# Performance work log

Measured on AMD Instinct MI355X. Metric: run time of the kernel, lower is better.

Reference implementation:

```python
import jax, jax.numpy as jnp
import numpy as np


def setup_inputs() -> dict:
    key = jax.random.key(0)
    kh, ks, kwi, kwo, kcw = jax.random.split(key, 5)
    B = 2048        # decode batch (one token per request)
    H = 2048        # hidden_size
    K = 4           # conv kernel; L_cache = K - 1 = 3
    P = 8192        # req_to_token_pool size
    hidden_states = jax.random.normal(kh, (B, H), dtype=jnp.float32)
    conv_state = jax.random.normal(ks, (P, H, K - 1), dtype=jnp.float32)
    # unique, in-range pool slots (index_copy_ semantics need uniqueness)
    req_pool_indices = jnp.arange(B, dtype=jnp.int32)
    w_in = jax.random.normal(kwi, (3 * H, H), dtype=jnp.float32) * 0.02
    w_out = jax.random.normal(kwo, (H, H), dtype=jnp.float32) * 0.02
    conv_w = jax.random.normal(kcw, (H, K), dtype=jnp.float32) * 0.2
    return {
        "hidden_states": hidden_states,
        "conv_state": conv_state,
        "req_pool_indices": req_pool_indices,
        "w_in": w_in,
        "w_out": w_out,
        "conv_w": conv_w,
    }


def reference(hidden_states, conv_state, req_pool_indices, w_in, w_out, conv_w):
    """Lfm2ShortConv._forward_decode (conv_bias=False).

    Returns (y, new_conv_state) where new_conv_state is the scattered cache.
    """
    idx = req_pool_indices.astype(jnp.int32)
    # in_proj: [B, H] @ [H, 3H] -> [B, 3H]
    proj = hidden_states @ w_in.T
    B_gate, C_gate, x = jnp.split(proj, 3, axis=-1)
    Bx = B_gate * x                                  # [B, H]
    cur = conv_state[idx]                            # gather: [B, H, K-1]
    # sliding window: [old state (K-1 taps), newest token] -> [B, H, K]
    conv_in = jnp.concatenate([cur, Bx[:, :, None]], axis=-1)
    # depthwise causal conv as mul-sum over taps
    conv_out = jnp.einsum("bhk,hk->bh", conv_in, conv_w)
    y = (C_gate * conv_out) @ w_out.T                # [B, H]
    # scatter updated window (drop oldest tap)
    new_conv_state = conv_state.at[idx].set(conv_in[:, :, 1:])
    return y, new_conv_state
```

## Files before the change

### kernel.cpp

```cpp
#include <hip/hip_runtime.h>
#include <hip/hip_bf16.h>


typedef __bf16 bf16x8 __attribute__((ext_vector_type(8)));
typedef float f32x4 __attribute__((ext_vector_type(4)));

__device__ __forceinline__ unsigned short f2bf(float f) {
    union { float f; unsigned int u; } c; c.f = f;
    unsigned int u = c.u;
    u = u + 0x7FFFu + ((u >> 16) & 1u);
    return (unsigned short)(u >> 16);
}
__device__ __forceinline__ float bf2f(unsigned short u) {
    union { unsigned int i; float f; } c; c.i = ((unsigned int)u) << 16;
    return c.f;
}

__global__ void prep(const float4* __restrict__ hs, const float4* __restrict__ wi,
                     const float4* __restrict__ wo,
                     ushort4* __restrict__ hs_bf, ushort4* __restrict__ wi_bf,
                     ushort4* __restrict__ wo_bf,
                     float4* __restrict__ y,
                     int* __restrict__ inv, int P,
                     int n1, int n2, int n3, int n4) {
    int i = blockIdx.x * blockDim.x + threadIdx.x;
    if (i < P) inv[i] = -1;
    const float4* s; ushort4* d; int j = i;
    if (j < n1)            { s = hs; d = hs_bf; }
    else if ((j -= n1) < n2) { s = wi; d = wi_bf; }
    else if ((j -= n2) < n3) { s = wo; d = wo_bf; }
    else if ((j -= n3) < n4) { float4 z = {0.f, 0.f, 0.f, 0.f}; y[j] = z; return; }
    else return;
    float4 v = s[j];
    ushort4 o; o.x = f2bf(v.x); o.y = f2bf(v.y); o.z = f2bf(v.z); o.w = f2bf(v.w);
    d[j] = o;
}

__global__ void scatter_inv(const int* __restrict__ idx, int* __restrict__ inv, int B) {
    int b = blockIdx.x * blockDim.x + threadIdx.x;
    if (b < B) inv[idx[b]] = b;
}


#define GTILE 128
#define GBK 64

__device__ __forceinline__ void gl_lds16(const unsigned short* g, unsigned short* l) {
    __builtin_amdgcn_global_load_lds(
        (const __attribute__((address_space(1))) unsigned int*)g,
        (__attribute__((address_space(3))) unsigned int*)l,
        16, 0, 0);
}

template<int MODE>
__global__ __launch_bounds__(256) void gemm_bt(
    const unsigned short* __restrict__ A,
    const unsigned short* __restrict__ B,
    void* __restrict__ Cv,
    int M, int N, int K, int ksplit, int nbx,
    const float* __restrict__ cs_in,
    const int* __restrict__ inv,
    float* __restrict__ cs_out,
    int HL, int P, int NC)
{
    __shared__ __align__(16) unsigned short Asm[GTILE * GBK];
    __shared__ __align__(16) unsigned short Bsm[GTILE * GBK];

    int bm, bn, kb;
    if (MODE == 1) {
        int id = blockIdx.x;
        int q = id / 5, r = id % 5;
        if (r == 4) {
            for (int p = q; p < P; p += NC) {
                if (inv[p] >= 0) continue;
                const float4* s4 = (const float4*)(cs_in + (size_t)p * HL);
                float4* d4 = (float4*)(cs_out + (size_t)p * HL);
#pragma unroll
                for (int f = threadIdx.x; f < GTILE * 12; f += 256) d4[f] = s4[f];
            }
            return;
        }
        int gid = q * 4 + r;
        bn = (gid % nbx) * GTILE;
        bm = (gid / nbx) * GTILE;
        kb = 0;
    } else {
        bn = blockIdx.x * GTILE;
        bm = blockIdx.y * GTILE;
        kb = blockIdx.z * ksplit;
    }

    const int tid  = threadIdx.x;
    const int lane = tid & 63;
    const int wave = tid >> 6;
    const int quad = lane >> 4;
    const int l16  = lane & 15;

    const int wm = (wave >> 1) * 64;
    const int wn = (wave & 1) * 64;

    f32x4 acc[4][4] = {};

    const int sr = tid >> 3;
    const int scsw = (((tid & 7) ^ (sr & 7)) * 8);
    const unsigned short* Ag[4];
    const unsigned short* Bg[4];
#pragma unroll
    for (int k4 = 0; k4 < 4; k4++) {
        Ag[k4] = A + (size_t)(bm + k4 * 32 + sr) * K + scsw;
        Bg[k4] = B + (size_t)(bn + k4 * 32 + sr) * K + scsw;
    }

    for (int kt = kb; kt < kb + ksplit; kt += GBK) {
        __syncthreads();
#pragma unroll
        for (int k4 = 0; k4 < 4; k4++) {
            gl_lds16(Ag[k4] + kt, Asm + k4 * 2048 + wave * 512);
            gl_lds16(Bg[k4] + kt, Bsm + k4 * 2048 + wave * 512);
        }
        __syncthreads();

#pragma unroll
        for (int kk = 0; kk < 2; kk++) {
            bf16x8 a[4], b[4];
            const int csw = (kk * 32 + quad * 8) ^ ((l16 & 7) * 8);
#pragma unroll
            for (int i = 0; i < 4; i++)
                a[i] = *(const bf16x8*)&Asm[(wm + i * 16 + l16) * GBK + csw];
#pragma unroll
            for (int j = 0; j < 4; j++)
                b[j] = *(const bf16x8*)&Bsm[(wn + j * 16 + l16) * GBK + csw];
#pragma unroll
            for (int i = 0; i < 4; i++)
#pragma unroll
                for (int j = 0; j < 4; j++)
                    acc[i][j] = __builtin_amdgcn_mfma_f32_16x16x32_bf16(
                        a[i], b[j], acc[i][j], 0, 0, 0);
        }
    }

#pragma unroll
    for (int i = 0; i < 4; i++) {
#pragma unroll
        for (int j = 0; j < 4; j++) {
#pragma unroll
            for (int r = 0; r < 4; r++) {
                int row = bm + wm + i * 16 + quad * 4 + r;
                int col = bn + wn + j * 16 + l16;
                if (MODE == 1) {
                    ((unsigned short*)Cv)[(size_t)row * N + col] = f2bf(acc[i][j][r]);
                } else {
                    __hip_atomic_fetch_add((float*)Cv + (size_t)row * N + col,
                                           acc[i][j][r],
                                           __ATOMIC_RELAXED,
                                           __HIP_MEMORY_SCOPE_AGENT);
                }
            }
        }
    }
}

__global__ void elemwise(const unsigned short* __restrict__ proj,
                         const float* __restrict__ cs_in,
                         const int* __restrict__ idx,
                         const float* __restrict__ conv_w,
                         float* __restrict__ state_out,
                         unsigned short* __restrict__ g_bf,
                         int B, int H, int hshift, int hmask)
{
    int t = blockIdx.x * blockDim.x + threadIdx.x;
    if (t >= B * H) return;
    int b = t >> hshift;
    int h = t & hmask;
    int slot = idx[b];
    size_t prow = (size_t)b * 3 * H;
    float Bg = bf2f(proj[prow + h]);
    float Cg = bf2f(proj[prow + H + h]);
    float xv = bf2f(proj[prow + 2 * H + h]);
    float bx = Bg * xv;
    const float* cs = cs_in + ((size_t)slot * H + h) * 3;
    float c0 = cs[0], c1 = cs[1], c2 = cs[2];
    float4 cw = *(const float4*)(conv_w + 4 * h);
    float co = c0 * cw.x + c1 * cw.y + c2 * cw.z + bx * cw.w;
    float* so = state_out + ((size_t)slot * H + h) * 3;
    so[0] = c1; so[1] = c2; so[2] = bx;
    g_bf[t] = f2bf(Cg * co);
}

extern "C" void kernel_launch(void* const* d_in, const int* in_sizes, int n_in,
                              void* d_out, int out_size, void* d_ws, size_t ws_size,
                              hipStream_t stream) {
    const float* hs         = (const float*)d_in[0];
    const float* conv_state = (const float*)d_in[1];
    const int*   idx        = (const int*)d_in[2];
    const float* w_in       = (const float*)d_in[3];
    const float* w_out      = (const float*)d_in[4];
    const float* conv_w     = (const float*)d_in[5];

    const int B  = in_sizes[2];
    const int H  = in_sizes[0] / B;
    const int Kc = in_sizes[5] / H;
    const int Lc = Kc - 1;
    const int P  = (int)((long long)in_sizes[1] / ((long long)H * Lc));

    float* y_out     = (float*)d_out;
    float* state_out = y_out + (size_t)B * H;

    unsigned short* hs_bf    = (unsigned short*)d_ws;
    unsigned short* w_in_bf  = hs_bf + (size_t)B * H;
    unsigned short* w_out_bf = w_in_bf + (size_t)3 * H * H;
    unsigned short* proj_bf  = w_out_bf + (size_t)H * H;
    unsigned short* g_bf     = proj_bf + (size_t)B * 3 * H;
    int*            inv      = (int*)(g_bf + (size_t)B * H);

    const int thr = 256;

    {
        int n1 = B * H / 4, n2 = 3 * H * H / 4, n3 = H * H / 4, n4 = B * H / 4;
        int tot = n1 + n2 + n3 + n4;
        prep<<<(tot + thr - 1) / thr, thr, 0, stream>>>(
            (const float4*)hs, (const float4*)w_in, (const float4*)w_out,
            (ushort4*)hs_bf, (ushort4*)w_in_bf, (ushort4*)w_out_bf,
            (float4*)y_out, inv, P, n1, n2, n3, n4);
    }
    scatter_inv<<<(B + thr - 1) / thr, thr, 0, stream>>>(idx, inv, B);

    {
        int nbx = 3 * H / GTILE;
        int NG  = nbx * (B / GTILE);
        int NC  = NG / 4;
        gemm_bt<1><<<NG + NC, 256, 0, stream>>>(
            hs_bf, w_in_bf, proj_bf, B, 3 * H, H, H, nbx,
            conv_state, inv, state_out, 3 * H, P, NC);
    }

    {
        int hshift = 0; while ((1 << hshift) < H) hshift++;
        int n = B * H;
        elemwise<<<(n + thr - 1) / thr, thr, 0, stream>>>(
            proj_bf, conv_state, idx, conv_w, state_out, g_bf, B, H, hshift, H - 1);
    }

    {
        dim3 grid(H / GTILE, B / GTILE, 4);
        gemm_bt<0><<<grid, 256, 0, stream>>>(
            g_bf, w_out_bf, y_out, B, H, H, H / 4, H / GTILE,
            nullptr, nullptr, nullptr, 0, 0, 0);
    }
}
```

Before: 579.5 us.

## Replace atomic split-K accumulation with partial buffers and reduction; batch state copies

The second GEMM now splits K in two instead of four and writes plain float partials into a workspace buffer instead of using atomic adds. A separate kernel then sums the two partials into the output, so prep no longer has to zero y. The conv-state copy blocks now handle two pool rows per iteration, issuing all loads before the stores to raise memory-level parallelism. The trade-offs are an extra kernel launch and extra partial-buffer traffic, plus fewer blocks in the second GEMM.

```diff
diff --git a/kernel.cpp b/kernel.cpp
--- a/kernel.cpp
+++ b/kernel.cpp
@@ -20,16 +20,14 @@
                      const float4* __restrict__ wo,
                      ushort4* __restrict__ hs_bf, ushort4* __restrict__ wi_bf,
                      ushort4* __restrict__ wo_bf,
-                     float4* __restrict__ y,
                      int* __restrict__ inv, int P,
-                     int n1, int n2, int n3, int n4) {
+                     int n1, int n2, int n3) {
     int i = blockIdx.x * blockDim.x + threadIdx.x;
     if (i < P) inv[i] = -1;
     const float4* s; ushort4* d; int j = i;
     if (j < n1)            { s = hs; d = hs_bf; }
     else if ((j -= n1) < n2) { s = wi; d = wi_bf; }
     else if ((j -= n2) < n3) { s = wo; d = wo_bf; }
-    else if ((j -= n3) < n4) { float4 z = {0.f, 0.f, 0.f, 0.f}; y[j] = z; return; }
     else return;
     float4 v = s[j];
     ushort4 o; o.x = f2bf(v.x); o.y = f2bf(v.y); o.z = f2bf(v.z); o.w = f2bf(v.w);
@@ -71,12 +69,32 @@
         int id = blockIdx.x;
         int q = id / 5, r = id % 5;
         if (r == 4) {
-            for (int p = q; p < P; p += NC) {
-                if (inv[p] >= 0) continue;
-                const float4* s4 = (const float4*)(cs_in + (size_t)p * HL);
-                float4* d4 = (float4*)(cs_out + (size_t)p * HL);
-#pragma unroll
-                for (int f = threadIdx.x; f < GTILE * 12; f += 256) d4[f] = s4[f];
+            const int t = threadIdx.x;
+            for (int p = q; p < P; p += 2 * NC) {
+                const int p1 = p + NC;
+                const int iv0 = inv[p];
+                const int iv1 = (p1 < P) ? inv[p1] : 0;
+                const float4* s0 = (const float4*)(cs_in + (size_t)p  * HL);
+                float4*       d0 = (float4*)(cs_out       + (size_t)p  * HL);
+                const float4* s1 = (const float4*)(cs_in + (size_t)p1 * HL);
+                float4*       d1 = (float4*)(cs_out       + (size_t)p1 * HL);
+                float4 t0[6], t1[6];
+                if (iv0 < 0) {
+#pragma unroll
+                    for (int u = 0; u < 6; u++) t0[u] = s0[t + u * 256];
+                }
+                if (iv1 < 0) {
+#pragma unroll
+                    for (int u = 0; u < 6; u++) t1[u] = s1[t + u * 256];
+                }
+                if (iv0 < 0) {
+#pragma unroll
+                    for (int u = 0; u < 6; u++) d0[t + u * 256] = t0[u];
+                }
+                if (iv1 < 0) {
+#pragma unroll
+                    for (int u = 0; u < 6; u++) d1[t + u * 256] = t1[u];
+                }
             }
             return;
         }
@@ -150,10 +168,8 @@
                 if (MODE == 1) {
                     ((unsigned short*)Cv)[(size_t)row * N + col] = f2bf(acc[i][j][r]);
                 } else {
-                    __hip_atomic_fetch_add((float*)Cv + (size_t)row * N + col,
-                                           acc[i][j][r],
-                                           __ATOMIC_RELAXED,
-                                           __HIP_MEMORY_SCOPE_AGENT);
+                    float* Cp = (float*)Cv + (size_t)blockIdx.z * M * N;
+                    Cp[(size_t)row * N + col] = acc[i][j][r];
                 }
             }
         }
@@ -187,6 +203,15 @@
     g_bf[t] = f2bf(Cg * co);
 }
 
+__global__ void reduce2(const float4* __restrict__ p0, const float4* __restrict__ p1,
+                        float4* __restrict__ y, int n4) {
+    int i = blockIdx.x * blockDim.x + threadIdx.x;
+    if (i >= n4) return;
+    float4 a = p0[i], b = p1[i];
+    float4 o; o.x = a.x + b.x; o.y = a.y + b.y; o.z = a.z + b.z; o.w = a.w + b.w;
+    y[i] = o;
+}
+
 extern "C" void kernel_launch(void* const* d_in, const int* in_sizes, int n_in,
                               void* d_out, int out_size, void* d_ws, size_t ws_size,
                               hipStream_t stream) {
@@ -211,17 +236,18 @@
     unsigned short* w_out_bf = w_in_bf + (size_t)3 * H * H;
     unsigned short* proj_bf  = w_out_bf + (size_t)H * H;
     unsigned short* g_bf     = proj_bf + (size_t)B * 3 * H;
-    int*            inv      = (int*)(g_bf + (size_t)B * H);
+    float*          part     = (float*)(g_bf + (size_t)B * H);
+    int*            inv      = (int*)(part + (size_t)2 * B * H);
 
     const int thr = 256;
 
     {
-        int n1 = B * H / 4, n2 = 3 * H * H / 4, n3 = H * H / 4, n4 = B * H / 4;
-        int tot = n1 + n2 + n3 + n4;
+        int n1 = B * H / 4, n2 = 3 * H * H / 4, n3 = H * H / 4;
+        int tot = n1 + n2 + n3;
         prep<<<(tot + thr - 1) / thr, thr, 0, stream>>>(
             (const float4*)hs, (const float4*)w_in, (const float4*)w_out,
             (ushort4*)hs_bf, (ushort4*)w_in_bf, (ushort4*)w_out_bf,
-            (float4*)y_out, inv, P, n1, n2, n3, n4);
+            inv, P, n1, n2, n3);
     }
     scatter_inv<<<(B + thr - 1) / thr, thr, 0, stream>>>(idx, inv, B);
 
@@ -242,9 +268,13 @@
     }
 
     {
-        dim3 grid(H / GTILE, B / GTILE, 4);
+        dim3 grid(H / GTILE, B / GTILE, 2);
         gemm_bt<0><<<grid, 256, 0, stream>>>(
-            g_bf, w_out_bf, y_out, B, H, H, H / 4, H / GTILE,
+            g_bf, w_out_bf, part, B, H, H, H / 2, H / GTILE,
             nullptr, nullptr, nullptr, 0, 0, 0);
-    }
-}
+        int n4 = B * H / 4;
+        reduce2<<<(n4 + thr - 1) / thr, thr, 0, stream>>>(
+            (const float4*)part, (const float4*)(part + (size_t)B * H),
+            (float4*)y_out, n4);
+    }
+}
```

Result: no change. 582.0 us (+0.4%).
